# Performance work log

Hardware: AMD Instinct MI355X
Metric: run time of the kernel (lower is better)

Reference implementation:

```python
import jax, jax.numpy as jnp
import numpy as np

N_QUBITS = 14
N_LAYERS = 4
N_CLASSES = 10
BATCH = 1024


def apply_1q(state, gate, wire):
    """Apply a 2x2 gate ([2,2] shared or [B,2,2] batched) to `wire` of state [B,2,...,2]."""
    s = jnp.moveaxis(state, wire + 1, -1)
    shp = s.shape
    s = s.reshape(shp[0], -1, 2)
    if gate.ndim == 3:
        s = jnp.einsum('bij,bkj->bki', gate, s)
    else:
        s = jnp.einsum('ij,bkj->bki', gate, s)
    return jnp.moveaxis(s.reshape(shp), -1, wire + 1)


def apply_cnot(state, c, t):
    s = jnp.moveaxis(state, (c + 1, t + 1), (-2, -1))
    s = jnp.stack([s[..., 0, :], s[..., 1, ::-1]], axis=-2)
    return jnp.moveaxis(s, (-2, -1), (c + 1, t + 1))


def simulate(x, q_params):
    """Batched statevector sim of: RY(x_i) embed -> BasicEntanglerLayers(RX + CNOT ring) -> <Z_i>."""
    B, n = x.shape
    state = jnp.zeros((B,) + (2,) * n, jnp.complex64)
    state = state.at[(slice(None),) + (0,) * n].set(1.0)

    # RY(x_i) on each wire (angles batched per sample)
    c, s = jnp.cos(0.5 * x), jnp.sin(0.5 * x)
    for w in range(n):
        g = jnp.stack([jnp.stack([c[:, w], -s[:, w]], -1),
                       jnp.stack([s[:, w], c[:, w]], -1)], -2).astype(jnp.complex64)  # [B,2,2]
        state = apply_1q(state, g, w)

    # BasicEntanglerLayers: per layer RX(weights[l,i]) on every wire, then CNOT ring
    cw, sw = jnp.cos(0.5 * q_params), jnp.sin(0.5 * q_params)
    n_layers = q_params.shape[0]
    for l in range(n_layers):
        for w in range(n):
            cc = cw[l, w].astype(jnp.complex64)
            isw = (-1j) * sw[l, w].astype(jnp.complex64)
            g = jnp.stack([jnp.stack([cc, isw]), jnp.stack([isw, cc])])  # [2,2] RX
            state = apply_1q(state, g, w)
        if n == 2:
            state = apply_cnot(state, 0, 1)
        else:
            for w in range(n):
                state = apply_cnot(state, w, (w + 1) % n)

    # <Z_i> = P(bit_i=0) - P(bit_i=1)
    p = jnp.abs(state) ** 2  # [B,2,...,2] real
    axes_all = tuple(range(1, n + 1))
    z = []
    for w in range(n):
        pw = jnp.sum(p, axis=tuple(a for a in axes_all if a != w + 1))  # [B,2]
        z.append(pw[:, 0] - pw[:, 1])
    return jnp.stack(z, -1).astype(jnp.float32)  # [B, n]


def setup_inputs() -> dict:
    key = jax.random.key(0)
    k1, k2, k3, k4 = jax.random.split(key, 4)
    x = jax.random.normal(k1, (BATCH, N_QUBITS), dtype=jnp.float32)
    q_params = 0.01 * jax.random.normal(k2, (N_LAYERS, N_QUBITS), dtype=jnp.float32)
    fc_w = jax.random.normal(k3, (N_CLASSES, N_QUBITS), dtype=jnp.float32) / np.sqrt(N_QUBITS)
    fc_b = jax.random.normal(k4, (N_CLASSES,), dtype=jnp.float32) * 0.01
    return {"x": x, "q_params": q_params, "fc_w": fc_w, "fc_b": fc_b}


def reference(x, q_params, fc_w, fc_b):
    q_out = simulate(x, q_params)            # [B, n_qubits]
    logits = q_out @ fc_w.T + fc_b           # [B, n_classes]
    return logits
```

## Files before the change

### kernel.cpp

```cpp
#include <hip/hip_runtime.h>
#include <hip/hip_fp16.h>
#include <math.h>


#define NQ 14
#define NLAYERS 4
#define NCLASSES 10
#define BLOCK 512

typedef _Float16 f16;
typedef _Float16 f16x2 __attribute__((ext_vector_type(2)));
typedef _Float16 f16x4 __attribute__((ext_vector_type(4)));
typedef _Float16 f16x8 __attribute__((ext_vector_type(8)));
typedef float f32x4 __attribute__((ext_vector_type(4)));
typedef unsigned int u32;
typedef u32 u32x2 __attribute__((ext_vector_type(2)));

__device__ __forceinline__ f32x4 mf(f16x8 a, f16x8 b, f32x4 c) {
  return __builtin_amdgcn_mfma_f32_16x16x32_f16(a, b, c, 0, 0, 0);
}
__device__ __forceinline__ f32x4 mf16(f16x4 a, f16x4 b, f32x4 c) {
  return __builtin_amdgcn_mfma_f32_16x16x16f16(a, b, c, 0, 0, 0);
}
__device__ __forceinline__ int swz(int t) { return ((t ^ (t >> 3)) & 7) << 3; }

__device__ __forceinline__ f16x4 cvt4(f32x4 v) {
  u32x2 r;
  r[0] = __builtin_bit_cast(u32, __builtin_amdgcn_cvt_pkrtz(v[0], v[1]));
  r[1] = __builtin_bit_cast(u32, __builtin_amdgcn_cvt_pkrtz(v[2], v[3]));
  return __builtin_bit_cast(f16x4, r);
}
__device__ __forceinline__ u32 dwof(f16x4 v, int k) {
  return __builtin_bit_cast(u32x2, v)[k];
}

__device__ __forceinline__ int finv5(int n) {
  n ^= ((n >> 3) & 1) << 4;
  n ^= ((n >> 2) & 1) << 3;
  n ^= ((n >> 1) & 1) << 2;
  n ^= (n & 1) << 1;
  return n;
}
__device__ __forceinline__ int finv3(int n) {
  n ^= ((n >> 2) & 1) << 3;
  n ^= ((n >> 1) & 1) << 2;
  n ^= (n & 1) << 1;
  return n;
}

__device__ __forceinline__ void build32(f16* Bc, const float* qc, const float* qs,
                                        int base, int tid) {
  const float c0 = qc[base], c1 = qc[base+1], c2 = qc[base+2], c3 = qc[base+3], c4 = qc[base+4];
  const float s0 = qs[base], s1 = qs[base+1], s2 = qs[base+2], s3 = qs[base+3], s4 = qs[base+4];
#pragma unroll
  for (int e = tid; e < 1024; e += BLOCK) {
    const int n = e >> 5, k = e & 31;
    const int d = finv5(n) ^ k;
    float mag = ((d & 1) ? s0 : c0) * ((d & 2) ? s1 : c1);
    mag *= ((d & 4) ? s2 : c2) * ((d & 8) ? s3 : c3);
    mag *= ((d & 16) ? s4 : c4);
    const int t = __popc(d) & 3;
    const f16 v = (f16)((t == 1 || t == 2) ? -mag : mag);
    const int p = 256 * (k >> 3) + 8 * n + (k & 7);
    const bool isreal = !(t & 1);
    Bc[p]        = isreal ? v : (f16)0.f;
    Bc[p + 1024] = isreal ? (f16)0.f : v;
  }
}

__device__ __forceinline__ void buildC2(f16* Cc, const float* qc, const float* qs,
                                        int base, int tid) {
  if (tid < 256) {
    const float c0 = qc[base], c1 = qc[base+1], c2 = qc[base+2], c3 = qc[base+3];
    const float s0 = qs[base], s1 = qs[base+1], s2 = qs[base+2], s3 = qs[base+3];
    const int rp = tid >> 4, k = tid & 15;
    const int d = finv3(rp) ^ k;
    float mag = ((d & 1) ? s0 : c0) * ((d & 2) ? s1 : c1);
    mag *= ((d & 4) ? s2 : c2) * ((d & 8) ? s3 : c3);
    const int t = __popc(d) & 3;
    const f16 v = (f16)((t == 1 || t == 2) ? -mag : mag);
    const bool isreal = !(t & 1);
    const int p = 16 * rp + k;
    Cc[p]       = isreal ? v : (f16)0.f;
    Cc[p + 256] = isreal ? (f16)0.f : v;
    Cc[p + 512] = isreal ? (f16)0.f : (f16)(-v);
  }
}

__device__ __forceinline__ void passA(f16* __restrict__ reP, f16* __restrict__ imP,
                                      const f16* __restrict__ BcR, int tid) {
  const int lane = tid & 63, wave = tid >> 6;
  const int q = lane >> 4, cc = lane & 15;
  const int n0 = cc, n1 = cc | 16;
  const f16x8 br0 = *(const f16x8*)(BcR + 256 * q + 8 * n0);
  const f16x8 bi0 = *(const f16x8*)(BcR + 1024 + 256 * q + 8 * n0);
  const f16x8 br1 = *(const f16x8*)(BcR + 256 * q + 8 * n1);
  const f16x8 bi1 = *(const f16x8*)(BcR + 1024 + 256 * q + 8 * n1);
  f16x4 outR[8], outI[8];
#pragma unroll
  for (int i = 0; i < 4; ++i) {
    const int mt = wave * 4 + i;
    const int pA = mt * 512 + ((128 * q + 8 * cc) ^ swz(mt));
    const f16x8 Ar = *(const f16x8*)(reP + pA);
    const f16x8 Ai = *(const f16x8*)(imP + pA);
    const f16x8 nAi = -Ai;
    {
      f32x4 aR = {0.f,0.f,0.f,0.f}, aI = {0.f,0.f,0.f,0.f};
      aR = mf(Ar, br0, aR); aR = mf(nAi, bi0, aR);
      aI = mf(Ar, bi0, aI); aI = mf(Ai, br0, aI);
      outR[i * 2 + 0] = cvt4(aR);
      outI[i * 2 + 0] = cvt4(aI);
    }
    {
      f32x4 aR = {0.f,0.f,0.f,0.f}, aI = {0.f,0.f,0.f,0.f};
      aR = mf(Ar, br1, aR); aR = mf(nAi, bi1, aR);
      aI = mf(Ar, bi1, aI); aI = mf(Ai, br1, aI);
      outR[i * 2 + 1] = cvt4(aR);
      outI[i * 2 + 1] = cvt4(aI);
    }
  }
  __syncthreads();
#pragma unroll
  for (int i = 0; i < 4; ++i) {
    const int mt = wave * 4 + i;
#pragma unroll
    for (int nt = 0; nt < 2; ++nt) {
      const int n5 = nt * 16 + cc;
      const int pS = n5 * 512 +
          ((128 * (2 * (mt & 1) + (q >> 1)) + 8 * (mt >> 1) + 4 * (q & 1)) ^ swz(n5));
      *(f16x4*)(reP + pS) = outR[i * 2 + nt];
      *(f16x4*)(imP + pS) = outI[i * 2 + nt];
    }
  }
}

template<bool FINAL>
__device__ __forceinline__ void superBC(f16* __restrict__ reP, f16* __restrict__ imP,
                                        const f16* __restrict__ BcR,
                                        const f16* __restrict__ Cc,
                                        int tid, float* __restrict__ zloc) {
  const int lane = tid & 63, wave = tid >> 6;
  const int q = lane >> 4, cc = lane & 15;
  int n0 = cc, n1 = cc | 16;
  if (wave >= 4) { n0 ^= 31; n1 ^= 31; }
  const f16x8 br0 = *(const f16x8*)(BcR + 256 * q + 8 * n0);
  const f16x8 bi0 = *(const f16x8*)(BcR + 1024 + 256 * q + 8 * n0);
  const f16x8 br1 = *(const f16x8*)(BcR + 256 * q + 8 * n1);
  const f16x8 bi1 = *(const f16x8*)(BcR + 1024 + 256 * q + 8 * n1);
  const int r0 = 16 * cc + 4 * q, r1 = 16 * (cc ^ 15) + 4 * q;
  const f16x4 ucr0 = *(const f16x4*)(Cc + r0);
  const f16x4 uci0 = *(const f16x4*)(Cc + 256 + r0);
  const f16x4 ucn0 = *(const f16x4*)(Cc + 512 + r0);
  const f16x4 ucr1 = *(const f16x4*)(Cc + r1);
  const f16x4 uci1 = *(const f16x4*)(Cc + 256 + r1);
  const f16x4 ucn1 = *(const f16x4*)(Cc + 512 + r1);

  f16x4 accR[4][2], accI[4][2];
  float z0b = 0.f, z1b = 0.f, z9b = 0.f, zA = 0.f, zB = 0.f, pt = 0.f;
#pragma unroll
  for (int i = 0; i < 4; ++i) {
    const int mt = wave * 4 + i;
    const int pA = mt * 512 + ((128 * q + 8 * cc) ^ swz(mt));
    const f16x8 Ar = *(const f16x8*)(reP + pA);
    const f16x8 Ai = *(const f16x8*)(imP + pA);
    const f16x8 nAi = -Ai;
#pragma unroll
    for (int h = 0; h < 2; ++h) {
      const f16x8 br = h ? br1 : br0;
      const f16x8 bi = h ? bi1 : bi0;
      f32x4 aR = {0.f,0.f,0.f,0.f}, aI = {0.f,0.f,0.f,0.f};
      aR = mf(Ar, br, aR); aR = mf(nAi, bi, aR);
      aI = mf(Ar, bi, aI); aI = mf(Ai, br, aI);
      const f16x4 s1r = cvt4(aR), s1i = cvt4(aI);
      const f16x4 ur = h ? ucr1 : ucr0;
      const f16x4 ui = h ? uci1 : uci0;
      const f16x4 un = h ? ucn1 : ucn0;
      f32x4 cR = {0.f,0.f,0.f,0.f}, cI = {0.f,0.f,0.f,0.f};
      cR = mf16(ur, s1r, cR); cR = mf16(un, s1i, cR);
      cI = mf16(ui, s1r, cI); cI = mf16(ur, s1i, cI);
      if constexpr (FINAL) {
        const float p0 = cR[0]*cR[0] + cI[0]*cI[0];
        const float p1 = cR[1]*cR[1] + cI[1]*cI[1];
        const float p2 = cR[2]*cR[2] + cI[2]*cI[2];
        const float p3 = cR[3]*cR[3] + cI[3]*cI[3];
        const float ps = (p0 + p1) + (p2 + p3);
        zA += (p0 - p1) + (p2 - p3);
        zB += (p0 + p1) - (p2 + p3);
        z0b += (i & 1) ? -ps : ps;
        z1b += (i & 2) ? -ps : ps;
        z9b += h ? -ps : ps;
        pt  += ps;
      } else {
        accR[i][h] = cvt4(cR);
        accI[i][h] = cvt4(cI);
      }
    }
  }
  if constexpr (FINAL) {
    zloc[0]  += (q & 2) ? -z0b : z0b;
    zloc[1]  += z1b;
    zloc[2]  += (wave & 1) ? -pt : pt;
    zloc[3]  += (wave & 2) ? -pt : pt;
    zloc[4]  += (wave & 4) ? -pt : pt;
    zloc[5]  += (cc & 1) ? -pt : pt;
    zloc[6]  += (cc & 2) ? -pt : pt;
    zloc[7]  += (cc & 4) ? -pt : pt;
    zloc[8]  += (cc & 8) ? -pt : pt;
    zloc[9]  += z9b;
    zloc[10] += zA;
    zloc[11] += zB;
    zloc[12] += (q & 1) ? -pt : pt;
    zloc[13] += (q & 2) ? -pt : pt;
  } else {
    __syncthreads();
    const u32 selLo = (q & 2) ? 0x01000504u : 0x05040100u;
    const u32 selHi = (q & 2) ? 0x03020706u : 0x07060302u;
    const int ibase = 128 * (wave >> 1) + 4 * (wave & 1);
#pragma unroll
    for (int h = 0; h < 2; ++h) {
#pragma unroll
      for (int j = 0; j < 4; ++j) {
        const int pS = (8 * q + 2 * j + h) * 512 + ibase +
                       8 * (cc ^ (2 * j + h) ^ q);
        const int dj = j >> 1;
        const u32 sel = (j & 1) ? selHi : selLo;
        u32x2 vr, vi;
        vr[0] = __builtin_amdgcn_perm(dwof(accR[1][h], dj), dwof(accR[0][h], dj), sel);
        vr[1] = __builtin_amdgcn_perm(dwof(accR[3][h], dj), dwof(accR[2][h], dj), sel);
        vi[0] = __builtin_amdgcn_perm(dwof(accI[1][h], dj), dwof(accI[0][h], dj), sel);
        vi[1] = __builtin_amdgcn_perm(dwof(accI[3][h], dj), dwof(accI[2][h], dj), sel);
        *(u32x2*)(reP + pS) = vr;
        *(u32x2*)(imP + pS) = vi;
      }
    }
  }
}

__global__ __launch_bounds__(BLOCK, 4) void qsim_kernel(
    const float* __restrict__ x, const float* __restrict__ qp,
    const float* __restrict__ fcw, const float* __restrict__ fcb,
    float* __restrict__ out) {
  extern __shared__ unsigned char smem[];
  f16* reP = (f16*)smem;
  f16* imP = reP + 16384;
  f16* Bc  = imP + 16384;
  f16* Cc  = Bc + 2048;
  float* qc = (float*)(Cc + 768);
  float* qs = qc + 56;
  float* xc = qs + 56;
  float* xs = xc + 14;

  const int b = blockIdx.x;
  const int tid = threadIdx.x;

  if (tid < NQ) {
    float sv, cv; sincosf(0.5f * x[b * NQ + tid], &sv, &cv);
    xc[tid] = cv; xs[tid] = sv;
  } else if (tid >= 64 && tid < 64 + NLAYERS * NQ) {
    const int k = tid - 64;
    float sv, cv; sincosf(0.5f * qp[k], &sv, &cv);
    qc[k] = cv; qs[k] = sv;
  }
  __syncthreads();

  float* Flo  = (float*)Bc;
  float* psi  = Flo + 32;
  float* PsiR = psi + 32;
  float* PsiI = PsiR + 32;
  if (tid < 32) {
    float f = 1.f;
#pragma unroll
    for (int j = 0; j < 5; ++j) f *= ((tid >> j) & 1) ? xs[5 + j] : xc[5 + j];
    Flo[tid] = f;
  } else if (tid < 64) {
    const int k = tid - 32;
    float f = 1.f;
#pragma unroll
    for (int j = 0; j < 5; ++j) f *= ((k >> j) & 1) ? xs[j] : xc[j];
    psi[k] = f;
  }
  __syncthreads();
  if (tid < 32) {
    const float c0 = qc[0], c1 = qc[1], c2 = qc[2], c3 = qc[3], c4 = qc[4];
    const float s0 = qs[0], s1 = qs[1], s2 = qs[2], s3 = qs[3], s4 = qs[4];
    const int a = finv5(tid);
    float ar = 0.f, ai = 0.f;
    for (int k = 0; k < 32; ++k) {
      const int d = a ^ k;
      float mag = ((d & 1) ? s0 : c0) * ((d & 2) ? s1 : c1);
      mag *= ((d & 4) ? s2 : c2) * ((d & 8) ? s3 : c3);
      mag *= ((d & 16) ? s4 : c4);
      mag *= psi[k];
      const int t = __popc(d) & 3;
      if (t == 0) ar += mag; else if (t == 1) ai -= mag;
      else if (t == 2) ar -= mag; else ai += mag;
    }
    PsiR[tid] = ar; PsiI[tid] = ai;
  }
  __syncthreads();
  {
    float fhi = 1.f;
#pragma unroll
    for (int j = 0; j < 4; ++j) fhi *= ((tid >> j) & 1) ? xs[10 + j] : xc[10 + j];
    const float cr = fhi * PsiR[tid >> 4], ci = fhi * PsiI[tid >> 4];
    const int t = tid >> 4;
    const int sz = swz(t);
    float Fl[32];
#pragma unroll
    for (int j = 0; j < 32; ++j) Fl[j] = Flo[j];
    __syncthreads();
#pragma unroll
    for (int kb = 0; kb < 4; ++kb) {
      f16x8 hr, hi;
#pragma unroll
      for (int j = 0; j < 8; ++j) {
        const float F = Fl[8 * kb + j];
        hr[j] = (f16)(F * cr);
        hi[j] = (f16)(F * ci);
      }
      const int pb = t * 512 + ((128 * kb + 8 * (tid & 15)) ^ sz);
      *(f16x8*)(reP + pb) = hr;
      *(f16x8*)(imP + pb) = hi;
    }
  }
  build32(Bc, qc, qs, 0 * NQ + 5, tid);
  buildC2(Cc, qc, qs, 0 * NQ + 10, tid);
  __syncthreads();

  superBC<false>(reP, imP, Bc, Cc, tid, nullptr);   __syncthreads();
#pragma unroll
  for (int l = 1; l < NLAYERS; ++l) {
    build32(Bc, qc, qs, l * NQ + 0, tid);           __syncthreads();
    passA(reP, imP, Bc, tid);                       __syncthreads();
    build32(Bc, qc, qs, l * NQ + 5, tid);
    buildC2(Cc, qc, qs, l * NQ + 10, tid);
    __syncthreads();
    if (l < NLAYERS - 1) {
      superBC<false>(reP, imP, Bc, Cc, tid, nullptr); __syncthreads();
    }
  }

  float zloc[NQ];
#pragma unroll
  for (int w = 0; w < NQ; ++w) zloc[w] = 0.f;
  superBC<true>(reP, imP, Bc, Cc, tid, zloc);
  __syncthreads();

  float* zpart = (float*)Bc;
  float* zbuf  = zpart + 112;
#pragma unroll
  for (int w = 0; w < NQ; ++w) {
#pragma unroll
    for (int off = 32; off > 0; off >>= 1)
      zloc[w] += __shfl_down(zloc[w], off, 64);
  }
  const int wave = tid >> 6, lane = tid & 63;
  if (lane == 0) {
#pragma unroll
    for (int w = 0; w < NQ; ++w) zpart[wave * NQ + w] = zloc[w];
  }
  __syncthreads();
  if (tid < NQ) {
    float a = 0.f;
#pragma unroll
    for (int v = 0; v < 8; ++v) a += zpart[v * NQ + tid];
    zbuf[tid] = a;
  }
  __syncthreads();
  if (tid < NCLASSES) {
    float acc = fcb[tid];
#pragma unroll
    for (int w = 0; w < NQ; ++w) acc = fmaf(zbuf[w], fcw[tid * NQ + w], acc);
    out[b * NCLASSES + tid] = acc;
  }
}

extern "C" void kernel_launch(void* const* d_in, const int* in_sizes, int n_in,
                              void* d_out, int out_size, void* d_ws, size_t ws_size,
                              hipStream_t stream) {
  const float* x   = (const float*)d_in[0];
  const float* qp  = (const float*)d_in[1];
  const float* fcw = (const float*)d_in[2];
  const float* fcb = (const float*)d_in[3];
  float* out = (float*)d_out;
  const int B = in_sizes[0] / NQ;

  const size_t shmem = (size_t)(2 * 16384 + 2048 + 768) * sizeof(f16)
                     + (size_t)(56 + 56 + 14 + 14) * sizeof(float);
  (void)hipFuncSetAttribute((const void*)qsim_kernel,
                            hipFuncAttributeMaxDynamicSharedMemorySize, (int)shmem);
  qsim_kernel<<<B, BLOCK, shmem, stream>>>(x, qp, fcw, fcb, out);
}
```

Baseline: 122.8 us.

## Double-buffer gate matrices and fold gate builds into passes to cut barriers

Adds a second shared-memory buffer for the 32x32 gate matrix so the next stage's gate matrix can be built while the current pass runs. The build32/buildC2 calls move into the tail of passA/superBC, and the separate barriers around them go away. Both passes now load their state tiles into registers first and then hit a single barrier before the MFMA work, replacing the old barrier between compute and store. This cuts the number of block-wide __syncthreads per layer, at the cost of extra shared memory and register pressure from holding four A tiles live.

```diff
diff --git a/kernel.cpp b/kernel.cpp
--- a/kernel.cpp
+++ b/kernel.cpp
@@ -88,7 +88,11 @@
 }
 
 __device__ __forceinline__ void passA(f16* __restrict__ reP, f16* __restrict__ imP,
-                                      const f16* __restrict__ BcR, int tid) {
+                                      const f16* __restrict__ BcR,
+                                      f16* __restrict__ BcW, int baseB,
+                                      f16* __restrict__ CcW, int baseC,
+                                      const float* __restrict__ qc,
+                                      const float* __restrict__ qs, int tid) {
   const int lane = tid & 63, wave = tid >> 6;
   const int q = lane >> 4, cc = lane & 15;
   const int n0 = cc, n1 = cc | 16;
@@ -96,30 +100,34 @@
   const f16x8 bi0 = *(const f16x8*)(BcR + 1024 + 256 * q + 8 * n0);
   const f16x8 br1 = *(const f16x8*)(BcR + 256 * q + 8 * n1);
   const f16x8 bi1 = *(const f16x8*)(BcR + 1024 + 256 * q + 8 * n1);
-  f16x4 outR[8], outI[8];
+  f16x8 Ar[4], Ai[4];
 #pragma unroll
   for (int i = 0; i < 4; ++i) {
     const int mt = wave * 4 + i;
     const int pA = mt * 512 + ((128 * q + 8 * cc) ^ swz(mt));
-    const f16x8 Ar = *(const f16x8*)(reP + pA);
-    const f16x8 Ai = *(const f16x8*)(imP + pA);
-    const f16x8 nAi = -Ai;
+    Ar[i] = *(const f16x8*)(reP + pA);
+    Ai[i] = *(const f16x8*)(imP + pA);
+  }
+  __syncthreads();
+  f16x4 outR[8], outI[8];
+#pragma unroll
+  for (int i = 0; i < 4; ++i) {
+    const f16x8 nAi = -Ai[i];
     {
       f32x4 aR = {0.f,0.f,0.f,0.f}, aI = {0.f,0.f,0.f,0.f};
-      aR = mf(Ar, br0, aR); aR = mf(nAi, bi0, aR);
-      aI = mf(Ar, bi0, aI); aI = mf(Ai, br0, aI);
+      aR = mf(Ar[i], br0, aR); aR = mf(nAi, bi0, aR);
+      aI = mf(Ar[i], bi0, aI); aI = mf(Ai[i], br0, aI);
       outR[i * 2 + 0] = cvt4(aR);
       outI[i * 2 + 0] = cvt4(aI);
     }
     {
       f32x4 aR = {0.f,0.f,0.f,0.f}, aI = {0.f,0.f,0.f,0.f};
-      aR = mf(Ar, br1, aR); aR = mf(nAi, bi1, aR);
-      aI = mf(Ar, bi1, aI); aI = mf(Ai, br1, aI);
+      aR = mf(Ar[i], br1, aR); aR = mf(nAi, bi1, aR);
+      aI = mf(Ar[i], bi1, aI); aI = mf(Ai[i], br1, aI);
       outR[i * 2 + 1] = cvt4(aR);
       outI[i * 2 + 1] = cvt4(aI);
     }
   }
-  __syncthreads();
 #pragma unroll
   for (int i = 0; i < 4; ++i) {
     const int mt = wave * 4 + i;
@@ -132,12 +140,17 @@
       *(f16x4*)(imP + pS) = outI[i * 2 + nt];
     }
   }
+  build32(BcW, qc, qs, baseB, tid);
+  buildC2(CcW, qc, qs, baseC, tid);
 }
 
 template<bool FINAL>
 __device__ __forceinline__ void superBC(f16* __restrict__ reP, f16* __restrict__ imP,
                                         const f16* __restrict__ BcR,
                                         const f16* __restrict__ Cc,
+                                        f16* __restrict__ BcW, int baseB,
+                                        const float* __restrict__ qc,
+                                        const float* __restrict__ qs,
                                         int tid, float* __restrict__ zloc) {
   const int lane = tid & 63, wave = tid >> 6;
   const int q = lane >> 4, cc = lane & 15;
@@ -154,23 +167,28 @@
   const f16x4 ucr1 = *(const f16x4*)(Cc + r1);
   const f16x4 uci1 = *(const f16x4*)(Cc + 256 + r1);
   const f16x4 ucn1 = *(const f16x4*)(Cc + 512 + r1);
-
-  f16x4 accR[4][2], accI[4][2];
-  float z0b = 0.f, z1b = 0.f, z9b = 0.f, zA = 0.f, zB = 0.f, pt = 0.f;
+  f16x8 Ar[4], Ai[4];
 #pragma unroll
   for (int i = 0; i < 4; ++i) {
     const int mt = wave * 4 + i;
     const int pA = mt * 512 + ((128 * q + 8 * cc) ^ swz(mt));
-    const f16x8 Ar = *(const f16x8*)(reP + pA);
-    const f16x8 Ai = *(const f16x8*)(imP + pA);
-    const f16x8 nAi = -Ai;
+    Ar[i] = *(const f16x8*)(reP + pA);
+    Ai[i] = *(const f16x8*)(imP + pA);
+  }
+  if constexpr (!FINAL) __syncthreads();
+
+  f16x4 accR[4][2], accI[4][2];
+  float z0b = 0.f, z1b = 0.f, z9b = 0.f, zA = 0.f, zB = 0.f, pt = 0.f;
+#pragma unroll
+  for (int i = 0; i < 4; ++i) {
+    const f16x8 nAi = -Ai[i];
 #pragma unroll
     for (int h = 0; h < 2; ++h) {
       const f16x8 br = h ? br1 : br0;
       const f16x8 bi = h ? bi1 : bi0;
       f32x4 aR = {0.f,0.f,0.f,0.f}, aI = {0.f,0.f,0.f,0.f};
-      aR = mf(Ar, br, aR); aR = mf(nAi, bi, aR);
-      aI = mf(Ar, bi, aI); aI = mf(Ai, br, aI);
+      aR = mf(Ar[i], br, aR); aR = mf(nAi, bi, aR);
+      aI = mf(Ar[i], bi, aI); aI = mf(Ai[i], br, aI);
       const f16x4 s1r = cvt4(aR), s1i = cvt4(aI);
       const f16x4 ur = h ? ucr1 : ucr0;
       const f16x4 ui = h ? uci1 : uci0;
@@ -212,7 +230,6 @@
     zloc[12] += (q & 1) ? -pt : pt;
     zloc[13] += (q & 2) ? -pt : pt;
   } else {
-    __syncthreads();
     const u32 selLo = (q & 2) ? 0x01000504u : 0x05040100u;
     const u32 selHi = (q & 2) ? 0x03020706u : 0x07060302u;
     const int ibase = 128 * (wave >> 1) + 4 * (wave & 1);
@@ -233,6 +250,7 @@
         *(u32x2*)(imP + pS) = vi;
       }
     }
+    build32(BcW, qc, qs, baseB, tid);
   }
 }
 
@@ -243,8 +261,9 @@
   extern __shared__ unsigned char smem[];
   f16* reP = (f16*)smem;
   f16* imP = reP + 16384;
-  f16* Bc  = imP + 16384;
-  f16* Cc  = Bc + 2048;
+  f16* Bc0 = imP + 16384;
+  f16* Bc1 = Bc0 + 2048;
+  f16* Cc  = Bc1 + 2048;
   float* qc = (float*)(Cc + 768);
   float* qs = qc + 56;
   float* xc = qs + 56;
@@ -263,7 +282,7 @@
   }
   __syncthreads();
 
-  float* Flo  = (float*)Bc;
+  float* Flo  = (float*)Bc0;
   float* psi  = Flo + 32;
   float* PsiR = psi + 32;
   float* PsiI = PsiR + 32;
@@ -323,30 +342,29 @@
       *(f16x8*)(imP + pb) = hi;
     }
   }
-  build32(Bc, qc, qs, 0 * NQ + 5, tid);
+  build32(Bc0, qc, qs, 0 * NQ + 5, tid);
   buildC2(Cc, qc, qs, 0 * NQ + 10, tid);
   __syncthreads();
 
-  superBC<false>(reP, imP, Bc, Cc, tid, nullptr);   __syncthreads();
+  superBC<false>(reP, imP, Bc0, Cc, Bc1, 1 * NQ + 0, qc, qs, tid, nullptr);
+  __syncthreads();
 #pragma unroll
   for (int l = 1; l < NLAYERS; ++l) {
-    build32(Bc, qc, qs, l * NQ + 0, tid);           __syncthreads();
-    passA(reP, imP, Bc, tid);                       __syncthreads();
-    build32(Bc, qc, qs, l * NQ + 5, tid);
-    buildC2(Cc, qc, qs, l * NQ + 10, tid);
+    passA(reP, imP, Bc1, Bc0, l * NQ + 5, Cc, l * NQ + 10, qc, qs, tid);
     __syncthreads();
     if (l < NLAYERS - 1) {
-      superBC<false>(reP, imP, Bc, Cc, tid, nullptr); __syncthreads();
+      superBC<false>(reP, imP, Bc0, Cc, Bc1, (l + 1) * NQ + 0, qc, qs, tid, nullptr);
+      __syncthreads();
     }
   }
 
   float zloc[NQ];
 #pragma unroll
   for (int w = 0; w < NQ; ++w) zloc[w] = 0.f;
-  superBC<true>(reP, imP, Bc, Cc, tid, zloc);
-  __syncthreads();
-
-  float* zpart = (float*)Bc;
+  superBC<true>(reP, imP, Bc0, Cc, nullptr, 0, qc, qs, tid, zloc);
+  __syncthreads();
+
+  float* zpart = (float*)Bc0;
   float* zbuf  = zpart + 112;
 #pragma unroll
   for (int w = 0; w < NQ; ++w) {
@@ -385,7 +403,7 @@
   float* out = (float*)d_out;
   const int B = in_sizes[0] / NQ;
 
-  const size_t shmem = (size_t)(2 * 16384 + 2048 + 768) * sizeof(f16)
+  const size_t shmem = (size_t)(2 * 16384 + 2 * 2048 + 768) * sizeof(f16)
                      + (size_t)(56 + 56 + 14 + 14) * sizeof(float);
   (void)hipFuncSetAttribute((const void*)qsim_kernel,
                             hipFuncAttributeMaxDynamicSharedMemorySize, (int)shmem);
```

Result: no change. 120.5 us (-1.9%).
